# Kernel tuning notes

Hardware: AMD Instinct MI355X
Metric: run time of the kernel (lower is better)

## Reference

```python
import jax, jax.numpy as jnp
import numpy as np

N_LABELS = 48
L = N_LABELS + 2            # labels + stop + start
START = N_LABELS + 1
STOP = N_LABELS
NEG = -10000.0
B, T = 512, 1024


def setup_inputs() -> dict:
    key = jax.random.key(0)
    k1, k2, k3 = jax.random.split(key, 3)
    feats = jax.random.normal(k1, (B, T, L), dtype=jnp.float32)
    lens = jax.random.randint(k2, (B,), 1, T + 1, dtype=jnp.int32)
    transitions = jax.random.normal(k3, (L, L), dtype=jnp.float32)
    return {"feats": feats, "lens": lens, "transitions": transitions}


def reference(feats, lens, transitions):
    # Viterbi decode (module's forward). feats: [B, T, L]
    b, t, l = feats.shape
    vit0 = jnp.full((b, l), NEG, feats.dtype).at[:, START].set(0.0)

    def step(carry, logit):
        vit, c = carry                                   # vit [B,L], c [B]
        scores = vit[:, None, :] + transitions[None, :, :]   # [B, to, from]
        vt_max = scores.max(2)                           # [B, L]
        ptr = scores.argmax(2)                           # [B, L] backpointers
        vit_nxt = vt_max + logit
        vit_new = jnp.where((c > 0)[:, None], vit_nxt, vit)
        # add stop transition exactly when this is the last real timestep
        vit_new = vit_new + jnp.where((c == 1)[:, None], transitions[STOP][None, :], 0.0)
        return (vit_new, c - 1), ptr

    (vit, _), pointers = jax.lax.scan(step, (vit0, lens), jnp.swapaxes(feats, 0, 1))
    scores = vit.max(1)                                  # [B]
    idx = vit.argmax(1)                                  # [B]

    barange = jnp.arange(b)

    def back(i, ptr):
        ni = ptr[barange, i]
        return ni, ni

    _, back_seq = jax.lax.scan(back, idx, pointers, reverse=True)  # back_seq[t] = idx after ptr_t
    # original drops the earliest backtracked index (belongs to the virtual start step)
    paths = jnp.concatenate([back_seq[1:], idx[None]], axis=0).T   # [B, T]
    return scores, paths
```

## Files before the change

kernel.cpp:

```cpp
#include <hip/hip_runtime.h>

typedef unsigned char u8;

#define TT 1024
#define BB 512
#define LL 50
#define STOPI 48
#define STARTI 49
#define NEGV -10000.0f


__global__ __launch_bounds__(256) void viterbi_fwd(
    const float* __restrict__ feats, const int* __restrict__ lens,
    const float* __restrict__ trans, float* __restrict__ out_scores,
    int* __restrict__ idx_ws, u8* __restrict__ ptr_ws)
{
    const int b    = blockIdx.x;
    const int tid  = threadIdx.x;
    const int lane = tid & 63;
    const int w    = __builtin_amdgcn_readfirstlane(tid >> 6);
    const int off  = w * 13;
    const int row  = (lane < LL) ? lane : (LL - 1);

    float trrv[13];
#pragma unroll
    for (int jj = 0; jj < 13; ++jj) {
        const int j = off + jj;
        trrv[jj] = (j < LL) ? trans[row * LL + j] : -1.0e5f;
    }
    const float tr_stop = trans[STOPI * LL + row];
    const int len = lens[b];
    const int nchunks = (len + 15) >> 4;

    float vit = (lane == STARTI) ? 0.0f : NEGV;

    __shared__ float  featbuf[1024];
    __shared__ float2 partial[2][4][64];

    const float* fb = feats + (size_t)b * (TT * LL);
    u8* pt = ptr_ws + (size_t)b * (TT * LL) + (size_t)row * TT;

    const int ld = (tid < 200) ? tid : 199;
    float4 nf = ((const float4*)fb)[ld];

#define SCAN13(BV, BI)                                                         \
    {                                                                          \
        float b0_ = -3.4e38f, b1_ = -3.4e38f;                                  \
        int   i0_ = off, i1_ = off + 7;                                        \
        _Pragma("unroll")                                                      \
        for (int jj = 0; jj < 7; ++jj) {                                       \
            const float s = __int_as_float(__builtin_amdgcn_readlane(          \
                                __float_as_int(vit), off + jj)) + trrv[jj];    \
            if (s > b0_) { b0_ = s; i0_ = off + jj; }                          \
        }                                                                      \
        _Pragma("unroll")                                                      \
        for (int jj = 7; jj < 13; ++jj) {                                      \
            const float s = __int_as_float(__builtin_amdgcn_readlane(          \
                                __float_as_int(vit), off + jj)) + trrv[jj];    \
            if (s > b1_) { b1_ = s; i1_ = off + jj; }                          \
        }                                                                      \
        if (b1_ > b0_) { b0_ = b1_; i0_ = i1_; }                               \
        (BV) = b0_; (BI) = i0_;                                                \
    }

#define COMBINE(PAR, BV, BI)                                                   \
    {                                                                          \
        const float2 p0 = (PAR)[0][lane];                                      \
        const float2 p1 = (PAR)[1][lane];                                      \
        const float2 p2 = (PAR)[2][lane];                                      \
        const float2 p3 = (PAR)[3][lane];                                      \
        (BV) = p0.x; (BI) = __float_as_int(p0.y);                              \
        if (p1.x > (BV)) { (BV) = p1.x; (BI) = __float_as_int(p1.y); }         \
        if (p2.x > (BV)) { (BV) = p2.x; (BI) = __float_as_int(p2.y); }         \
        if (p3.x > (BV)) { (BV) = p3.x; (BI) = __float_as_int(p3.y); }         \
    }

    unsigned pk = 0;
    for (int c = 0; c < nchunks; ++c) {
        if (tid < 200) ((float4*)featbuf)[tid] = nf;
        {
            const int cn = (c + 1 > 63) ? 63 : c + 1;
            nf = ((const float4*)(fb + cn * 800))[ld];
        }
        asm volatile("s_waitcnt lgkmcnt(0)" ::: "memory");
        __builtin_amdgcn_s_barrier();
        asm volatile("" ::: "memory");

#pragma unroll
        for (int i = 0; i < 16; ++i) {
            const int t = (c << 4) + i;
            const float f = featbuf[i * 50 + lane];

            float bw; int iw;
            SCAN13(bw, iw)

            partial[t & 1][w][lane] = make_float2(bw, __int_as_float(iw));
            asm volatile("s_waitcnt lgkmcnt(0)" ::: "memory");
            __builtin_amdgcn_s_barrier();
            asm volatile("" ::: "memory");

            float bv; int bi;
            COMBINE(partial[t & 1], bv, bi)

            if (w == 0) {
                pk = (pk >> 8) | ((unsigned)bi << 24);
                if ((t & 3) == 3 && lane < LL)
                    *(unsigned*)(pt + t - 3) = pk;
            }

            if (t < len) {
                float nv = bv + f;
                if (t == len - 1) nv += tr_stop;
                vit = nv;
            }
        }
    }

    {
        float bw; int iw;
        SCAN13(bw, iw)
        partial[0][w][lane] = make_float2(bw, __int_as_float(iw));
        asm volatile("s_waitcnt lgkmcnt(0)" ::: "memory");
        __builtin_amdgcn_s_barrier();
        asm volatile("" ::: "memory");

        float bv; int bi;
        COMBINE(partial[0], bv, bi)

        const unsigned pat = (unsigned)bi * 0x01010101u;
        uint4 q; q.x = pat; q.y = pat; q.z = pat; q.w = pat;
        if (lane < LL)
            for (int c2 = nchunks + w; c2 < 64; c2 += 4)
                *(uint4*)(pt + (c2 << 4)) = q;
    }

    if (w == 0) {
        float m = -3.4e38f; int mi = 0;
#pragma unroll
        for (int j = 0; j < LL; ++j) {
            float s = __int_as_float(__builtin_amdgcn_readlane(__float_as_int(vit), j));
            if (s > m) { m = s; mi = j; }
        }
        if (lane == 0) { out_scores[b] = m; idx_ws[b] = mi; }
    }
#undef SCAN13
#undef COMBINE
}

__global__ __launch_bounds__(64) void viterbi_bwd(
    const int* __restrict__ idx_ws, const u8* __restrict__ ptr_ws,
    float* __restrict__ out_paths)
{
    const int b = blockIdx.x;
    const int lane = threadIdx.x;

    __shared__ u8 lptr[TT * LL];
    __shared__ u8 maps[32 * LL];
    __shared__ int entries[33];

    {
        const uint4* src = (const uint4*)(ptr_ws + (size_t)b * TT * LL);
        uint4* dst = (uint4*)lptr;
        for (int i = lane; i < (TT * LL) / 16; i += 64) dst[i] = src[i];
    }
    __syncthreads();

    {
        int st[25], tt[25], cidx[25];
#pragma unroll
        for (int k = 0; k < 25; ++k) {
            int w = k * 64 + lane;
            int c = w / 50;
            int l = w - c * 50;
            st[k] = l;
            tt[k] = c * 32 + 31;
            cidx[k] = c * 50 + l;
        }
        for (int j = 0; j < 32; ++j) {
#pragma unroll
            for (int k = 0; k < 25; ++k) {
                st[k] = lptr[(st[k] << 10) + tt[k]];
                tt[k] -= 1;
            }
        }
#pragma unroll
        for (int k = 0; k < 25; ++k) maps[cidx[k]] = (u8)st[k];
    }
    __syncthreads();

    const int idx = idx_ws[b];

    if (lane == 0) {
        int i = idx;
        for (int c = 31; c >= 0; --c) {
            entries[c + 1] = i;
            i = maps[c * 50 + i];
        }
        entries[0] = i;
    }
    __syncthreads();

    float* po = out_paths + (size_t)b * TT;
    if (lane < 32) {
        const int c = lane;
        int s = entries[c + 1];
        for (int j = 0; j < 32; ++j) {
            int t = c * 32 + 31 - j;
            int ni = lptr[(s << 10) + t];
            if (t > 0) po[t - 1] = (float)ni;
            s = ni;
        }
    }
    if (lane == 0) po[TT - 1] = (float)idx;
}

extern "C" void kernel_launch(void* const* d_in, const int* in_sizes, int n_in,
                              void* d_out, int out_size, void* d_ws, size_t ws_size,
                              hipStream_t stream) {
    const float* feats = (const float*)d_in[0];
    const int*   lens  = (const int*)d_in[1];
    const float* trans = (const float*)d_in[2];

    float* scores = (float*)d_out;
    float* paths  = scores + BB;

    int* idx_ws = (int*)d_ws;
    u8*  ptr_ws = (u8*)d_ws + 4096;

    viterbi_fwd<<<BB, 256, 0, stream>>>(feats, lens, trans, scores, idx_ws, ptr_ws);
    viterbi_bwd<<<BB, 64, 0, stream>>>(idx_ws, ptr_ws, paths);
}
```

Baseline: 604.2 us.

## Split Viterbi forward into max-only recurrence and parallel backpointer recomputation

The serial forward pass now runs on a single wave per batch. It computes only the max (a tree of fmaxf, no argmax and no cross-wave barriers) and stores every timestep's Viterbi vector to workspace. A second, fully parallel kernel recomputes the argmax backpointers from the stored vectors for each (batch, 8-timestep) tile. The backward kernel also XOR-swizzles its LDS layout to cut bank conflicts. The cost is about 100 MB of extra global writes and reads, and a fallback to the old kernel when the workspace is too small.

```diff
diff --git a/kernel.cpp b/kernel.cpp
--- a/kernel.cpp
+++ b/kernel.cpp
@@ -9,8 +9,214 @@
 #define STARTI 49
 #define NEGV -10000.0f
 
-
-__global__ __launch_bounds__(256) void viterbi_fwd(
+#define PTR_OFF   4096
+#define PTR_BYTES ((size_t)BB * TT * LL)
+#define VIT_OFF   (PTR_OFF + PTR_BYTES)
+#define VIT_BYTES ((size_t)BB * TT * LL * 4)
+#define NEED_WS   (VIT_OFF + VIT_BYTES)
+
+#define MAX50(A, M)                                                            \
+    {                                                                          \
+        float r0_[17];                                                         \
+        _Pragma("unroll")                                                      \
+        for (int k_ = 0; k_ < 16; ++k_)                                        \
+            r0_[k_] = fmaxf(fmaxf((A)[3*k_], (A)[3*k_+1]), (A)[3*k_+2]);       \
+        r0_[16] = fmaxf((A)[48], (A)[49]);                                     \
+        float r1_[6];                                                          \
+        _Pragma("unroll")                                                      \
+        for (int k_ = 0; k_ < 5; ++k_)                                         \
+            r1_[k_] = fmaxf(fmaxf(r0_[3*k_], r0_[3*k_+1]), r0_[3*k_+2]);       \
+        r1_[5] = fmaxf(r0_[15], r0_[16]);                                      \
+        (M) = fmaxf(fmaxf(fmaxf(r1_[0], r1_[1]), r1_[2]),                      \
+                    fmaxf(fmaxf(r1_[3], r1_[4]), r1_[5]));                     \
+    }
+
+__global__ __launch_bounds__(64) void viterbi_max(
+    const float* __restrict__ feats, const int* __restrict__ lens,
+    const float* __restrict__ trans, float* __restrict__ out_scores,
+    int* __restrict__ idx_ws, float* __restrict__ vit_ws)
+{
+    const int b    = blockIdx.x;
+    const int lane = threadIdx.x;
+    if (lane >= LL) return;
+
+    float trr[LL];
+#pragma unroll
+    for (int j = 0; j < LL; ++j) trr[j] = trans[lane * LL + j];
+    const float tr_stop = trans[STOPI * LL + lane];
+    const int len = lens[b];
+
+    float vit = (lane == STARTI) ? 0.0f : NEGV;
+
+    const float* fb  = feats  + (size_t)b * (TT * LL);
+    float*       vst = vit_ws + (size_t)b * (TT * LL);
+
+    float f0 = fb[0 * LL + lane];
+    float f1 = fb[1 * LL + lane];
+    float f2 = fb[2 * LL + lane];
+    float f3 = fb[3 * LL + lane];
+
+#define K1STEP(T, F)                                                           \
+    {                                                                          \
+        if ((T) < len) {                                                       \
+            vst[(size_t)(T) * LL + lane] = vit;    \
+            const float fc_ = (F);                                             \
+            { int tp_ = (T) + 4; if (tp_ > TT - 1) tp_ = TT - 1;               \
+              (F) = fb[(size_t)tp_ * LL + lane]; }                             \
+            float a_[LL];                                                      \
+            _Pragma("unroll")                                                  \
+            for (int j_ = 0; j_ < LL; ++j_)                                    \
+                a_[j_] = __int_as_float(__builtin_amdgcn_readlane(             \
+                             __float_as_int(vit), j_)) + trr[j_];              \
+            float m_; MAX50(a_, m_)                                            \
+            float nv_ = m_ + fc_;                                              \
+            if ((T) == len - 1) nv_ += tr_stop;                                \
+            vit = nv_;                                                         \
+        }                                                                      \
+    }
+
+    const int nq = (len + 3) >> 2;
+    for (int q = 0; q < nq; ++q) {
+        const int tb = q << 2;
+        K1STEP(tb + 0, f0)
+        K1STEP(tb + 1, f1)
+        K1STEP(tb + 2, f2)
+        K1STEP(tb + 3, f3)
+    }
+#undef K1STEP
+
+    if (len < TT) vst[(size_t)len * LL + lane] = vit;
+
+    float m = -3.4e38f; int mi = 0;
+#pragma unroll
+    for (int j = 0; j < LL; ++j) {
+        float s = __int_as_float(__builtin_amdgcn_readlane(__float_as_int(vit), j));
+        if (s > m) { m = s; mi = j; }
+    }
+    if (lane == 0) { out_scores[b] = m; idx_ws[b] = mi; }
+}
+
+__global__ __launch_bounds__(256) void viterbi_ptr(
+    const int* __restrict__ lens, const float* __restrict__ trans,
+    const float* __restrict__ vit_ws, u8* __restrict__ ptr_ws)
+{
+    const int tid  = threadIdx.x;
+    const int lane = tid & 63;
+    if (lane >= LL) return;
+    const int wid = (blockIdx.x << 2) | (tid >> 6);
+    const int b   = wid >> 7;
+    const int t0  = (wid & 127) << 3;
+
+    float trr[LL];
+#pragma unroll
+    for (int j = 0; j < LL; ++j) trr[j] = trans[lane * LL + j];
+    const int len = lens[b];
+
+    const float* vbase = vit_ws + (size_t)b * (TT * LL);
+    u8* pt = ptr_ws + (size_t)b * (TT * LL) + (size_t)lane * TT;
+
+    unsigned pk0 = 0, pk1 = 0;
+    int prev_r = -1, idx = 0;
+#pragma unroll
+    for (int g = 0; g < 8; ++g) {
+        const int t = t0 + g;
+        const int r = (t < len) ? t : len;
+        if (r != prev_r) {
+            prev_r = r;
+            const float v = vbase[(size_t)r * LL + lane];
+            float a[LL];
+#pragma unroll
+            for (int j = 0; j < LL; ++j)
+                a[j] = __int_as_float(__builtin_amdgcn_readlane(
+                           __float_as_int(v), j)) + trr[j];
+            float m; MAX50(a, m)
+            int ii = 0;
+#pragma unroll
+            for (int j = LL - 1; j >= 0; --j)
+                if (a[j] == m) ii = j;
+            idx = ii;
+        }
+        if (g < 4) pk0 |= ((unsigned)idx) << (8 * g);
+        else       pk1 |= ((unsigned)idx) << (8 * (g - 4));
+    }
+    *(unsigned*)(pt + t0)     = pk0;
+    *(unsigned*)(pt + t0 + 4) = pk1;
+}
+
+#define LSW(S, T) (((S) << 10) + ((T) ^ (((S) & 31) << 2)))
+
+__global__ __launch_bounds__(64) void viterbi_bwd(
+    const int* __restrict__ idx_ws, const u8* __restrict__ ptr_ws,
+    float* __restrict__ out_paths)
+{
+    const int b = blockIdx.x;
+    const int lane = threadIdx.x;
+
+    __shared__ u8 lptr[TT * LL];
+    __shared__ u8 maps[32 * LL];
+    __shared__ int entries[33];
+
+    {
+        const unsigned* src = (const unsigned*)(ptr_ws + (size_t)b * TT * LL);
+        unsigned* dst = (unsigned*)lptr;
+        for (int i = lane; i < (TT * LL) / 4; i += 64) {
+            const int to = i >> 8;
+            const int t4 = i & 255;
+            dst[(to << 8) + (t4 ^ (to & 31))] = src[i];
+        }
+    }
+    __syncthreads();
+
+    {
+        int st[25], tt[25], cidx[25];
+#pragma unroll
+        for (int k = 0; k < 25; ++k) {
+            int w = k * 64 + lane;
+            int c = w / 50;
+            int l = w - c * 50;
+            st[k] = l;
+            tt[k] = c * 32 + 31;
+            cidx[k] = c * 50 + l;
+        }
+        for (int j = 0; j < 32; ++j) {
+#pragma unroll
+            for (int k = 0; k < 25; ++k) {
+                st[k] = lptr[LSW(st[k], tt[k])];
+                tt[k] -= 1;
+            }
+        }
+#pragma unroll
+        for (int k = 0; k < 25; ++k) maps[cidx[k]] = (u8)st[k];
+    }
+    __syncthreads();
+
+    const int idx = idx_ws[b];
+
+    if (lane == 0) {
+        int i = idx;
+        for (int c = 31; c >= 0; --c) {
+            entries[c + 1] = i;
+            i = maps[c * 50 + i];
+        }
+        entries[0] = i;
+    }
+    __syncthreads();
+
+    float* po = out_paths + (size_t)b * TT;
+    if (lane < 32) {
+        const int c = lane;
+        int s = entries[c + 1];
+        for (int j = 0; j < 32; ++j) {
+            int t = c * 32 + 31 - j;
+            int ni = lptr[LSW(s, t)];
+            if (t > 0) po[t - 1] = (float)ni;
+            s = ni;
+        }
+    }
+    if (lane == 0) po[TT - 1] = (float)idx;
+}
+
+__global__ __launch_bounds__(256) void viterbi_fwd_fb(
     const float* __restrict__ feats, const int* __restrict__ lens,
     const float* __restrict__ trans, float* __restrict__ out_scores,
     int* __restrict__ idx_ws, u8* __restrict__ ptr_ws)
@@ -62,7 +268,6 @@
         if (b1_ > b0_) { b0_ = b1_; i0_ = i1_; }                               \
         (BV) = b0_; (BI) = i0_;                                                \
     }
-
 #define COMBINE(PAR, BV, BI)                                                   \
     {                                                                          \
         const float2 p0 = (PAR)[0][lane];                                      \
@@ -107,7 +312,6 @@
                 if ((t & 3) == 3 && lane < LL)
                     *(unsigned*)(pt + t - 3) = pk;
             }
-
             if (t < len) {
                 float nv = bv + f;
                 if (t == len - 1) nv += tr_stop;
@@ -115,7 +319,6 @@
             }
         }
     }
-
     {
         float bw; int iw;
         SCAN13(bw, iw)
@@ -123,17 +326,14 @@
         asm volatile("s_waitcnt lgkmcnt(0)" ::: "memory");
         __builtin_amdgcn_s_barrier();
         asm volatile("" ::: "memory");
-
         float bv; int bi;
         COMBINE(partial[0], bv, bi)
-
         const unsigned pat = (unsigned)bi * 0x01010101u;
         uint4 q; q.x = pat; q.y = pat; q.z = pat; q.w = pat;
         if (lane < LL)
             for (int c2 = nchunks + w; c2 < 64; c2 += 4)
                 *(uint4*)(pt + (c2 << 4)) = q;
     }
-
     if (w == 0) {
         float m = -3.4e38f; int mi = 0;
 #pragma unroll
@@ -145,73 +345,6 @@
     }
 #undef SCAN13
 #undef COMBINE
-}
-
-__global__ __launch_bounds__(64) void viterbi_bwd(
-    const int* __restrict__ idx_ws, const u8* __restrict__ ptr_ws,
-    float* __restrict__ out_paths)
-{
-    const int b = blockIdx.x;
-    const int lane = threadIdx.x;
-
-    __shared__ u8 lptr[TT * LL];
-    __shared__ u8 maps[32 * LL];
-    __shared__ int entries[33];
-
-    {
-        const uint4* src = (const uint4*)(ptr_ws + (size_t)b * TT * LL);
-        uint4* dst = (uint4*)lptr;
-        for (int i = lane; i < (TT * LL) / 16; i += 64) dst[i] = src[i];
-    }
-    __syncthreads();
-
-    {
-        int st[25], tt[25], cidx[25];
-#pragma unroll
-        for (int k = 0; k < 25; ++k) {
-            int w = k * 64 + lane;
-            int c = w / 50;
-            int l = w - c * 50;
-            st[k] = l;
-            tt[k] = c * 32 + 31;
-            cidx[k] = c * 50 + l;
-        }
-        for (int j = 0; j < 32; ++j) {
-#pragma unroll
-            for (int k = 0; k < 25; ++k) {
-                st[k] = lptr[(st[k] << 10) + tt[k]];
-                tt[k] -= 1;
-            }
-        }
-#pragma unroll
-        for (int k = 0; k < 25; ++k) maps[cidx[k]] = (u8)st[k];
-    }
-    __syncthreads();
-
-    const int idx = idx_ws[b];
-
-    if (lane == 0) {
-        int i = idx;
-        for (int c = 31; c >= 0; --c) {
-            entries[c + 1] = i;
-            i = maps[c * 50 + i];
-        }
-        entries[0] = i;
-    }
-    __syncthreads();
-
-    float* po = out_paths + (size_t)b * TT;
-    if (lane < 32) {
-        const int c = lane;
-        int s = entries[c + 1];
-        for (int j = 0; j < 32; ++j) {
-            int t = c * 32 + 31 - j;
-            int ni = lptr[(s << 10) + t];
-            if (t > 0) po[t - 1] = (float)ni;
-            s = ni;
-        }
-    }
-    if (lane == 0) po[TT - 1] = (float)idx;
 }
 
 extern "C" void kernel_launch(void* const* d_in, const int* in_sizes, int n_in,
@@ -225,8 +358,14 @@
     float* paths  = scores + BB;
 
     int* idx_ws = (int*)d_ws;
-    u8*  ptr_ws = (u8*)d_ws + 4096;
-
-    viterbi_fwd<<<BB, 256, 0, stream>>>(feats, lens, trans, scores, idx_ws, ptr_ws);
+    u8*  ptr_ws = (u8*)d_ws + PTR_OFF;
+
+    if (ws_size >= NEED_WS) {
+        float* vit_ws = (float*)((u8*)d_ws + VIT_OFF);
+        viterbi_max<<<BB, 64, 0, stream>>>(feats, lens, trans, scores, idx_ws, vit_ws);
+        viterbi_ptr<<<(BB * 128) / 4, 256, 0, stream>>>(lens, trans, vit_ws, ptr_ws);
+    } else {
+        viterbi_fwd_fb<<<BB, 256, 0, stream>>>(feats, lens, trans, scores, idx_ws, ptr_ws);
+    }
     viterbi_bwd<<<BB, 64, 0, stream>>>(idx_ws, ptr_ws, paths);
 }
```

New measurement: 787.1 us. 1.3x slower.

## Split Viterbi forward into max-only producer wave and argmax consumer waves

Applied to the files above, without the earlier changes.

The forward kernel is restructured so one wave runs the serial recurrence with a max-only reduction, each lane holding a full transition row and reading the previous scores from a shared ring buffer. Two other waves recompute argmax backpointers from that ring one step behind and write them out, which takes the argmax and cross-wave combine off the serial critical path and cuts barriers to one per 8 steps. The backward kernel also gets an XOR-swizzled LDS layout for the pointer table to reduce bank conflicts. The cost is duplicated score computation, more registers per lane (launch bounds 192,2), and reliance on a 16-entry ring whose timing must stay correct across the barriers.

```diff
diff --git a/kernel.cpp b/kernel.cpp
--- a/kernel.cpp
+++ b/kernel.cpp
@@ -9,8 +9,83 @@
 #define STARTI 49
 #define NEGV -10000.0f
 
-
-__global__ __launch_bounds__(256) void viterbi_fwd(
+#define PTR_OFF 4096
+
+#define ROW_ADDS(ROWP, S, TRR)                                                 \
+    {                                                                          \
+        _Pragma("unroll")                                                      \
+        for (int k_ = 0; k_ < 13; ++k_) {                                      \
+            const float4 q_ = *(const float4*)((ROWP) + 4 * k_);               \
+            const int j_ = 4 * k_;                                             \
+            (S)[j_ + 0] = q_.x + (TRR)[j_ + 0];                                \
+            (S)[j_ + 1] = q_.y + (TRR)[j_ + 1];                                \
+            if (j_ + 2 < LL) (S)[j_ + 2] = q_.z + (TRR)[j_ + 2];               \
+            if (j_ + 3 < LL) (S)[j_ + 3] = q_.w + (TRR)[j_ + 3];               \
+        }                                                                      \
+    }
+
+#define MAX50(S, M)                                                            \
+    {                                                                          \
+        float r0_[17];                                                         \
+        _Pragma("unroll")                                                      \
+        for (int k_ = 0; k_ < 16; ++k_)                                        \
+            r0_[k_] = fmaxf(fmaxf((S)[3*k_], (S)[3*k_+1]), (S)[3*k_+2]);       \
+        r0_[16] = fmaxf((S)[48], (S)[49]);                                     \
+        float r1_[6];                                                          \
+        _Pragma("unroll")                                                      \
+        for (int k_ = 0; k_ < 5; ++k_)                                         \
+            r1_[k_] = fmaxf(fmaxf(r0_[3*k_], r0_[3*k_+1]), r0_[3*k_+2]);       \
+        r1_[5] = fmaxf(r0_[15], r0_[16]);                                      \
+        (M) = fmaxf(fmaxf(fmaxf(r1_[0], r1_[1]), r1_[2]),                      \
+                    fmaxf(fmaxf(r1_[3], r1_[4]), r1_[5]));                     \
+    }
+
+#define ARGMAX50(S, BI)                                                        \
+    {                                                                          \
+        float b0_=-3.4e38f, b1_=-3.4e38f, b2_=-3.4e38f, b3_=-3.4e38f;          \
+        int   i0_=0, i1_=13, i2_=26, i3_=39;                                   \
+        _Pragma("unroll")                                                      \
+        for (int j_=0;  j_<13; ++j_){ const float v_=(S)[j_]; if (v_>b0_){b0_=v_;i0_=j_;} } \
+        _Pragma("unroll")                                                      \
+        for (int j_=13; j_<26; ++j_){ const float v_=(S)[j_]; if (v_>b1_){b1_=v_;i1_=j_;} } \
+        _Pragma("unroll")                                                      \
+        for (int j_=26; j_<39; ++j_){ const float v_=(S)[j_]; if (v_>b2_){b2_=v_;i2_=j_;} } \
+        _Pragma("unroll")                                                      \
+        for (int j_=39; j_<50; ++j_){ const float v_=(S)[j_]; if (v_>b3_){b3_=v_;i3_=j_;} } \
+        if (b1_>b0_){b0_=b1_;i0_=i1_;}                                         \
+        if (b2_>b0_){b0_=b2_;i0_=i2_;}                                         \
+        if (b3_>b0_){b0_=b3_;i0_=i3_;}                                         \
+        (BI) = i0_;                                                            \
+    }
+
+#define PROCESS_GROUP(BASE)                                                    \
+    {                                                                          \
+        if (!have && (BASE) + 3 > len) {                                       \
+            const float* rowp_ = &ring[len & 15][0];                           \
+            float s_[LL];                                                      \
+            ROW_ADDS(rowp_, s_, trr)                                           \
+            ARGMAX50(s_, cidx)                                                 \
+            have = true;                                                       \
+        }                                                                      \
+        unsigned pk_ = 0;                                                      \
+        _Pragma("unroll 1")                                                    \
+        for (int r_ = 0; r_ < 4; ++r_) {                                       \
+            const int t_ = (BASE) + r_;                                        \
+            int idx_;                                                          \
+            if (t_ <= len) {                                                   \
+                const float* rowp_ = &ring[t_ & 15][0];                        \
+                float s_[LL];                                                  \
+                ROW_ADDS(rowp_, s_, trr)                                       \
+                ARGMAX50(s_, idx_)                                             \
+            } else {                                                           \
+                idx_ = cidx;                                                   \
+            }                                                                  \
+            pk_ |= (unsigned)idx_ << (8 * r_);                                 \
+        }                                                                      \
+        if (lane < LL) *(unsigned*)(pt + (BASE)) = pk_;                        \
+    }
+
+__global__ __launch_bounds__(192, 2) void viterbi_fused(
     const float* __restrict__ feats, const int* __restrict__ lens,
     const float* __restrict__ trans, float* __restrict__ out_scores,
     int* __restrict__ idx_ws, u8* __restrict__ ptr_ws)
@@ -19,133 +94,77 @@
     const int tid  = threadIdx.x;
     const int lane = tid & 63;
     const int w    = __builtin_amdgcn_readfirstlane(tid >> 6);
-    const int off  = w * 13;
     const int row  = (lane < LL) ? lane : (LL - 1);
 
-    float trrv[13];
-#pragma unroll
-    for (int jj = 0; jj < 13; ++jj) {
-        const int j = off + jj;
-        trrv[jj] = (j < LL) ? trans[row * LL + j] : -1.0e5f;
-    }
-    const float tr_stop = trans[STOPI * LL + row];
+    __shared__ float ring[16][64];
+
+    float trr[LL];
+#pragma unroll
+    for (int j = 0; j < LL; ++j) trr[j] = trans[row * LL + j];
     const int len = lens[b];
-    const int nchunks = (len + 15) >> 4;
-
-    float vit = (lane == STARTI) ? 0.0f : NEGV;
-
-    __shared__ float  featbuf[1024];
-    __shared__ float2 partial[2][4][64];
-
-    const float* fb = feats + (size_t)b * (TT * LL);
-    u8* pt = ptr_ws + (size_t)b * (TT * LL) + (size_t)row * TT;
-
-    const int ld = (tid < 200) ? tid : 199;
-    float4 nf = ((const float4*)fb)[ld];
-
-#define SCAN13(BV, BI)                                                         \
-    {                                                                          \
-        float b0_ = -3.4e38f, b1_ = -3.4e38f;                                  \
-        int   i0_ = off, i1_ = off + 7;                                        \
-        _Pragma("unroll")                                                      \
-        for (int jj = 0; jj < 7; ++jj) {                                       \
-            const float s = __int_as_float(__builtin_amdgcn_readlane(          \
-                                __float_as_int(vit), off + jj)) + trrv[jj];    \
-            if (s > b0_) { b0_ = s; i0_ = off + jj; }                          \
-        }                                                                      \
-        _Pragma("unroll")                                                      \
-        for (int jj = 7; jj < 13; ++jj) {                                      \
-            const float s = __int_as_float(__builtin_amdgcn_readlane(          \
-                                __float_as_int(vit), off + jj)) + trrv[jj];    \
-            if (s > b1_) { b1_ = s; i1_ = off + jj; }                          \
-        }                                                                      \
-        if (b1_ > b0_) { b0_ = b1_; i0_ = i1_; }                               \
-        (BV) = b0_; (BI) = i0_;                                                \
-    }
-
-#define COMBINE(PAR, BV, BI)                                                   \
-    {                                                                          \
-        const float2 p0 = (PAR)[0][lane];                                      \
-        const float2 p1 = (PAR)[1][lane];                                      \
-        const float2 p2 = (PAR)[2][lane];                                      \
-        const float2 p3 = (PAR)[3][lane];                                      \
-        (BV) = p0.x; (BI) = __float_as_int(p0.y);                              \
-        if (p1.x > (BV)) { (BV) = p1.x; (BI) = __float_as_int(p1.y); }         \
-        if (p2.x > (BV)) { (BV) = p2.x; (BI) = __float_as_int(p2.y); }         \
-        if (p3.x > (BV)) { (BV) = p3.x; (BI) = __float_as_int(p3.y); }         \
-    }
-
-    unsigned pk = 0;
-    for (int c = 0; c < nchunks; ++c) {
-        if (tid < 200) ((float4*)featbuf)[tid] = nf;
-        {
-            const int cn = (c + 1 > 63) ? 63 : c + 1;
-            nf = ((const float4*)(fb + cn * 800))[ld];
-        }
-        asm volatile("s_waitcnt lgkmcnt(0)" ::: "memory");
-        __builtin_amdgcn_s_barrier();
-        asm volatile("" ::: "memory");
-
-#pragma unroll
-        for (int i = 0; i < 16; ++i) {
-            const int t = (c << 4) + i;
-            const float f = featbuf[i * 50 + lane];
-
-            float bw; int iw;
-            SCAN13(bw, iw)
-
-            partial[t & 1][w][lane] = make_float2(bw, __int_as_float(iw));
+
+    if (w == 0) {
+        const float tr_stop = trans[STOPI * LL + row];
+        float vit = (lane == STARTI) ? 0.0f : NEGV;
+        const float* fb = feats + (size_t)b * (TT * LL);
+
+        float f[8];
+#pragma unroll
+        for (int i = 0; i < 8; ++i) f[i] = fb[i * LL + row];
+
+        for (int it = 0; it < 128; ++it) {
+#pragma unroll
+            for (int i = 0; i < 8; ++i) {
+                const int t = (it << 3) + i;
+                float* rowp = &ring[t & 15][0];
+                if (t <= len) {
+                    if (lane < LL) rowp[lane] = vit;
+                }
+                if (t < len) {
+                    float s[LL];
+                    ROW_ADDS(rowp, s, trr)
+                    float m; MAX50(s, m)
+                    float nv = m + f[i];
+                    if (t == len - 1) nv += tr_stop;
+                    vit = nv;
+                    int tp = t + 8; if (tp > TT - 1) tp = TT - 1;
+                    f[i] = fb[(size_t)tp * LL + row];
+                }
+            }
             asm volatile("s_waitcnt lgkmcnt(0)" ::: "memory");
             __builtin_amdgcn_s_barrier();
             asm volatile("" ::: "memory");
-
-            float bv; int bi;
-            COMBINE(partial[t & 1], bv, bi)
-
-            if (w == 0) {
-                pk = (pk >> 8) | ((unsigned)bi << 24);
-                if ((t & 3) == 3 && lane < LL)
-                    *(unsigned*)(pt + t - 3) = pk;
+        }
+
+        float m = -3.4e38f; int mi = 0;
+#pragma unroll
+        for (int j = 0; j < LL; ++j) {
+            float sv = __int_as_float(__builtin_amdgcn_readlane(__float_as_int(vit), j));
+            if (sv > m) { m = sv; mi = j; }
+        }
+        if (lane == 0) { out_scores[b] = m; idx_ws[b] = mi; }
+    } else {
+        u8* pt = ptr_ws + (size_t)b * (TT * LL) + (size_t)row * TT;
+        int  cidx = 0;
+        bool have = false;
+
+        for (int it = 0; it < 128; ++it) {
+            if (it > 0) {
+                const int base = ((it - 1) << 3) + ((w - 1) << 2);
+                PROCESS_GROUP(base)
             }
-
-            if (t < len) {
-                float nv = bv + f;
-                if (t == len - 1) nv += tr_stop;
-                vit = nv;
-            }
-        }
-    }
-
-    {
-        float bw; int iw;
-        SCAN13(bw, iw)
-        partial[0][w][lane] = make_float2(bw, __int_as_float(iw));
-        asm volatile("s_waitcnt lgkmcnt(0)" ::: "memory");
-        __builtin_amdgcn_s_barrier();
-        asm volatile("" ::: "memory");
-
-        float bv; int bi;
-        COMBINE(partial[0], bv, bi)
-
-        const unsigned pat = (unsigned)bi * 0x01010101u;
-        uint4 q; q.x = pat; q.y = pat; q.z = pat; q.w = pat;
-        if (lane < LL)
-            for (int c2 = nchunks + w; c2 < 64; c2 += 4)
-                *(uint4*)(pt + (c2 << 4)) = q;
-    }
-
-    if (w == 0) {
-        float m = -3.4e38f; int mi = 0;
-#pragma unroll
-        for (int j = 0; j < LL; ++j) {
-            float s = __int_as_float(__builtin_amdgcn_readlane(__float_as_int(vit), j));
-            if (s > m) { m = s; mi = j; }
-        }
-        if (lane == 0) { out_scores[b] = m; idx_ws[b] = mi; }
-    }
-#undef SCAN13
-#undef COMBINE
+            asm volatile("s_waitcnt lgkmcnt(0)" ::: "memory");
+            __builtin_amdgcn_s_barrier();
+            asm volatile("" ::: "memory");
+        }
+        {
+            const int base = (127 << 3) + ((w - 1) << 2);
+            PROCESS_GROUP(base)
+        }
+    }
 }
+
+#define LSW(S, T) (((S) << 10) + ((T) ^ (((S) & 31) << 2)))
 
 __global__ __launch_bounds__(64) void viterbi_bwd(
     const int* __restrict__ idx_ws, const u8* __restrict__ ptr_ws,
@@ -159,9 +178,13 @@
     __shared__ int entries[33];
 
     {
-        const uint4* src = (const uint4*)(ptr_ws + (size_t)b * TT * LL);
-        uint4* dst = (uint4*)lptr;
-        for (int i = lane; i < (TT * LL) / 16; i += 64) dst[i] = src[i];
+        const unsigned* src = (const unsigned*)(ptr_ws + (size_t)b * TT * LL);
+        unsigned* dst = (unsigned*)lptr;
+        for (int i = lane; i < (TT * LL) / 4; i += 64) {
+            const int to = i >> 8;
+            const int t4 = i & 255;
+            dst[(to << 8) + (t4 ^ (to & 31))] = src[i];
+        }
     }
     __syncthreads();
 
@@ -169,9 +192,9 @@
         int st[25], tt[25], cidx[25];
 #pragma unroll
         for (int k = 0; k < 25; ++k) {
-            int w = k * 64 + lane;
-            int c = w / 50;
-            int l = w - c * 50;
+            int ww = k * 64 + lane;
+            int c = ww / 50;
+            int l = ww - c * 50;
             st[k] = l;
             tt[k] = c * 32 + 31;
             cidx[k] = c * 50 + l;
@@ -179,7 +202,7 @@
         for (int j = 0; j < 32; ++j) {
 #pragma unroll
             for (int k = 0; k < 25; ++k) {
-                st[k] = lptr[(st[k] << 10) + tt[k]];
+                st[k] = lptr[LSW(st[k], tt[k])];
                 tt[k] -= 1;
             }
         }
@@ -206,7 +229,7 @@
         int s = entries[c + 1];
         for (int j = 0; j < 32; ++j) {
             int t = c * 32 + 31 - j;
-            int ni = lptr[(s << 10) + t];
+            int ni = lptr[LSW(s, t)];
             if (t > 0) po[t - 1] = (float)ni;
             s = ni;
         }
@@ -225,8 +248,8 @@
     float* paths  = scores + BB;
 
     int* idx_ws = (int*)d_ws;
-    u8*  ptr_ws = (u8*)d_ws + 4096;
-
-    viterbi_fwd<<<BB, 256, 0, stream>>>(feats, lens, trans, scores, idx_ws, ptr_ws);
+    u8*  ptr_ws = (u8*)d_ws + PTR_OFF;
+
+    viterbi_fused<<<BB, 192, 0, stream>>>(feats, lens, trans, scores, idx_ws, ptr_ws);
     viterbi_bwd<<<BB, 64, 0, stream>>>(idx_ws, ptr_ws, paths);
 }
```

After: 570.2 us. 1.06x faster.
